# Kernel optimization log

Measured on AMD Instinct MI355X. Metric: run time of the kernel, lower is better.

The kernel has to match this reference:

```python
import jax, jax.numpy as jnp
import numpy as np

TIMESTEPS = 1000
ZERO_W = 1.0
NONZERO_W = 1.0
VT_W = 1.0
VX_W = 1.0
VY_W = 1.0


def _holographic_transform(x, timesteps, transpose):
    """x: (B,1,H,W) -> (B,1,H,timesteps).
    For each nonzero pixel (h,w) with value v, write w (the column index) at
    time bin q = int(v*timesteps)-1 (negative q wraps, as torch's x[-1]=...).
    Torch iterates nonzeros in row-major order so on collisions the largest
    column index wins -> scatter-max reproduces that deterministically.
    """
    img = x[:, 0]
    if transpose:  # virtual_dim == 'x'
        img = jnp.swapaxes(img, 1, 2)
    B, H, W = img.shape
    q = (img * timesteps).astype(jnp.int32) - 1
    # zeros -> out-of-range index `timesteps`, dropped by mode='drop';
    # nonzeros: wrap -1 -> timesteps-1 like torch negative indexing
    q = jnp.where(img != 0, q % timesteps, timesteps)
    ycoord = jnp.broadcast_to(jnp.arange(W, dtype=x.dtype), (B, H, W))
    b_idx = jnp.arange(B)[:, None, None]
    h_idx = jnp.arange(H)[None, :, None]
    out = jnp.zeros((B, H, timesteps), x.dtype)
    out = out.at[b_idx, h_idx, q].max(ycoord, mode='drop')
    return out[:, None]


def _acb_mse(recon, target, zero_w, nonzero_w):
    zero_mask = target == 0
    d2 = (recon - target) ** 2
    c0 = zero_mask.sum()
    c1 = (~zero_mask).sum()
    # mean over each class; empty class (NaN in torch) -> 0
    l0 = jnp.where(c0 > 0, jnp.where(zero_mask, d2, 0.0).sum() / jnp.maximum(c0, 1), 0.0)
    l1 = jnp.where(c1 > 0, jnp.where(zero_mask, 0.0, d2).sum() / jnp.maximum(c1, 1), 0.0)
    return zero_w * l0 + nonzero_w * l1


def setup_inputs() -> dict:
    key = jax.random.key(0)
    k1, k2, k3, k4 = jax.random.split(key, 4)
    B, H, W = 32, 512, 512

    def sparse_img(kv, km):
        v = jax.random.uniform(kv, (B, 1, H, W), dtype=jnp.float32)
        keep = jax.random.uniform(km, (B, 1, H, W)) < 0.05
        return jnp.where(keep, v, 0.0)

    return {
        "reconstructed_image": sparse_img(k1, k2),
        "target_image": sparse_img(k3, k4),
    }


def reference(reconstructed_image, target_image):
    vt = _acb_mse(reconstructed_image, target_image, ZERO_W, NONZERO_W) * VT_W

    rx = _holographic_transform(reconstructed_image, TIMESTEPS, transpose=True)
    tx = _holographic_transform(target_image, TIMESTEPS, transpose=True)
    vx = _acb_mse(rx, tx, ZERO_W, NONZERO_W) * VX_W

    ry = _holographic_transform(reconstructed_image, TIMESTEPS, transpose=False)
    ty = _holographic_transform(target_image, TIMESTEPS, transpose=False)
    vy = _acb_mse(ry, ty, ZERO_W, NONZERO_W) * VY_W

    return vt + vx + vy
```

## Files before the change

### kernel.cpp

```cpp
#include <hip/hip_runtime.h>

#define TS 1000

__device__ __forceinline__ double wred(double v) {
#pragma unroll
    for (int o = 32; o > 0; o >>= 1) v += __shfl_down(v, o, 64);
    return v;
}

__device__ __forceinline__ void scat(unsigned* bins, float v, unsigned val) {
    if (v != 0.0f) {
        int q = (int)(v * 1000.0f) - 1;
        if (q < 0) q += TS;
        atomicMax(&bins[q], val);
    }
}

__global__ void kinit(double* acc, int n) {
    int i = blockIdx.x * blockDim.x + threadIdx.x;
    if (i < n) acc[i] = 0.0;
}

__global__ __launch_bounds__(256, 4) void kmain(const float* __restrict__ R,
                                                const float* __restrict__ T,
                                                double* __restrict__ acc,
                                                int ncopy_mask) {
    __shared__ unsigned bins[8000];
    const int tid = threadIdx.x;
    const uint4 z4 = make_uint4(0u, 0u, 0u, 0u);

    {
        uint4* p = (uint4*)bins;
        for (int i = tid; i < 2000; i += 256) p[i] = z4;
    }
    __syncthreads();

    const int lane = tid & 63, wv = tid >> 6;
    const int id = blockIdx.x;
    double* accrow = acc + (size_t)(id & ncopy_mask) * 16;

    double s0 = 0.0, ssum = 0.0;
    int c1 = 0;

    if ((id & 1) == 0) {
        const int kid = id >> 1;
        double t0 = 0.0, tsum = 0.0;
        int tc1 = 0;
        unsigned* bR = bins + wv * 2000;
        unsigned* bT = bR + 1000;
        uint4* r4 = (uint4*)bR;
        uint4* t4 = (uint4*)bT;
        for (int it = 0; it < 4; it++) {
            const size_t row = (size_t)kid * 16 + (size_t)(wv * 4 + it);
            const float4* R4 = (const float4*)(R + row * 512);
            const float4* T4 = (const float4*)(T + row * 512);
#pragma unroll
            for (int k = 0; k < 2; k++) {
                const int c = lane + k * 64;
                float4 rv = R4[c];
                float4 tv = T4[c];
                float rr[4] = {rv.x, rv.y, rv.z, rv.w};
                float tt[4] = {tv.x, tv.y, tv.z, tv.w};
#pragma unroll
                for (int j = 0; j < 4; j++) {
                    float a = rr[j], b = tt[j];
                    float d = a - b, d2 = d * d;
                    bool bz = (b == 0.0f);
                    tsum += (double)d2;
                    t0 += bz ? (double)d2 : 0.0;
                    tc1 += bz ? 0 : 1;
                    scat(bR, a, (unsigned)(c * 4 + j));
                    scat(bT, b, (unsigned)(c * 4 + j));
                }
            }
            __syncthreads();
            for (int g = lane; g < 250; g += 64) {
                uint4 rg = r4[g], tg = t4[g];
                r4[g] = z4;
                t4[g] = z4;
                if (rg.x | rg.y | rg.z | rg.w | tg.x | tg.y | tg.z | tg.w) {
                    unsigned ru[4] = {rg.x, rg.y, rg.z, rg.w};
                    unsigned tu[4] = {tg.x, tg.y, tg.z, tg.w};
#pragma unroll
                    for (int j = 0; j < 4; j++) {
                        float rb = (float)ru[j], tb = (float)tu[j];
                        float d = rb - tb, d2 = d * d;
                        bool tz = (tb == 0.0f);
                        ssum += (double)d2;
                        s0 += tz ? (double)d2 : 0.0;
                        c1 += tz ? 0 : 1;
                    }
                }
            }
            __syncthreads();
        }
        double v0 = wred(t0), v1 = wred(tsum), v2 = wred((double)tc1);
        double v3 = wred(s0), v4 = wred(ssum), v5 = wred((double)c1);
        if (lane == 0) {
            atomicAdd(&accrow[0], v0);
            atomicAdd(&accrow[1], v1);
            atomicAdd(&accrow[2], v2);
            atomicAdd(&accrow[3], v3);
            atomicAdd(&accrow[4], v4);
            atomicAdd(&accrow[5], v5);
        }
    } else {
        const int kid = id >> 1;
        const int b = kid >> 5;
        const int line = kid & 31;
        const float* Rb = R + (size_t)b * (512 * 512) + (size_t)line * 16;
        const float* Tb = T + (size_t)b * (512 * 512) + (size_t)line * 16;

        float4 ra[8], ta[8];
#pragma unroll
        for (int k = 0; k < 8; k++) {
            const int h = k * 64 + (tid >> 2);
            const int sub = (tid + k) & 3;
            const size_t off = (size_t)h * 512 + sub * 4;
            ra[k] = *(const float4*)(Rb + off);
            ta[k] = *(const float4*)(Tb + off);
        }

        uint4* r4 = (uint4*)bins;
        uint4* t4 = (uint4*)(bins + 4000);
#pragma unroll
        for (int p = 0; p < 4; p++) {
#pragma unroll
            for (int k = 0; k < 8; k++) {
                if (((tid + k) & 3) == p) {
                    const unsigned h = (unsigned)(k * 64 + (tid >> 2));
                    scat(bins + 0 * 1000, ra[k].x, h);
                    scat(bins + 1 * 1000, ra[k].y, h);
                    scat(bins + 2 * 1000, ra[k].z, h);
                    scat(bins + 3 * 1000, ra[k].w, h);
                    scat(bins + 4000 + 0 * 1000, ta[k].x, h);
                    scat(bins + 4000 + 1 * 1000, ta[k].y, h);
                    scat(bins + 4000 + 2 * 1000, ta[k].z, h);
                    scat(bins + 4000 + 3 * 1000, ta[k].w, h);
                }
            }
            __syncthreads();
            for (int g = tid; g < 1000; g += 256) {
                uint4 rg = r4[g], tg = t4[g];
                r4[g] = z4;
                t4[g] = z4;
                if (rg.x | rg.y | rg.z | rg.w | tg.x | tg.y | tg.z | tg.w) {
                    unsigned ru[4] = {rg.x, rg.y, rg.z, rg.w};
                    unsigned tu[4] = {tg.x, tg.y, tg.z, tg.w};
#pragma unroll
                    for (int j = 0; j < 4; j++) {
                        float rb = (float)ru[j], tb = (float)tu[j];
                        float d = rb - tb, d2 = d * d;
                        bool tz = (tb == 0.0f);
                        ssum += (double)d2;
                        s0 += tz ? (double)d2 : 0.0;
                        c1 += tz ? 0 : 1;
                    }
                }
            }
            __syncthreads();
        }
        double v3 = wred(s0), v4 = wred(ssum), v5 = wred((double)c1);
        if (lane == 0) {
            atomicAdd(&accrow[6], v3);
            atomicAdd(&accrow[7], v4);
            atomicAdd(&accrow[8], v5);
        }
    }
}

__global__ void kfin(const double* __restrict__ acc, float* __restrict__ out,
                     int ncopy) {
    const int lane = threadIdx.x;
    double v[9];
#pragma unroll
    for (int k = 0; k < 9; k++) v[k] = 0.0;
    if (lane < ncopy) {
#pragma unroll
        for (int k = 0; k < 9; k++) v[k] = acc[(size_t)lane * 16 + k];
    }
#pragma unroll
    for (int k = 0; k < 9; k++) {
#pragma unroll
        for (int o = 16; o > 0; o >>= 1) v[k] += __shfl_down(v[k], o, 64);
    }
    if (lane == 0) {
        const double NT = 8388608.0;
        const double NB = 16384000.0;
        double vt_c1 = v[2], vy_c1 = v[5], vx_c1 = v[8];
        double vt_c0 = NT - vt_c1, vy_c0 = NB - vy_c1, vx_c0 = NB - vx_c1;
        double vt_s1 = v[1] - v[0];
        double vy_s1 = v[4] - v[3];
        double vx_s1 = v[7] - v[6];
        double vt = (vt_c0 > 0.0 ? v[0] / vt_c0 : 0.0) +
                    (vt_c1 > 0.0 ? vt_s1 / vt_c1 : 0.0);
        double vy = (vy_c0 > 0.0 ? v[3] / vy_c0 : 0.0) +
                    (vy_c1 > 0.0 ? vy_s1 / vy_c1 : 0.0);
        double vx = (vx_c0 > 0.0 ? v[6] / vx_c0 : 0.0) +
                    (vx_c1 > 0.0 ? vx_s1 / vx_c1 : 0.0);
        out[0] = (float)(vt + vx + vy);
    }
}

extern "C" void kernel_launch(void* const* d_in, const int* in_sizes, int n_in,
                              void* d_out, int out_size, void* d_ws, size_t ws_size,
                              hipStream_t stream) {
    const float* R = (const float*)d_in[0];
    const float* T = (const float*)d_in[1];
    double* acc = (double*)d_ws;
    float* out = (float*)d_out;

    int ncopy = 16;
    while (ncopy > 1 && (size_t)ncopy * 16 * sizeof(double) > ws_size) ncopy >>= 1;

    hipLaunchKernelGGL(kinit, dim3(1), dim3(256), 0, stream, acc, ncopy * 16);
    hipLaunchKernelGGL(kmain, dim3(2048), dim3(256), 0, stream, R, T, acc, ncopy - 1);
    hipLaunchKernelGGL(kfin, dim3(1), dim3(64), 0, stream, acc, out, ncopy);
}
```

Before: 77.02 us.

## Drop block barriers in row path, prefetch rows, split double accumulators

Row-path blocks now let each wavefront zero and use its own private bin region. Block-wide barriers are replaced by per-wave lgkmcnt waits, and the next row's global loads are prefetched while the current row is scattered. Bins are cleared only when non-empty and not on the last pass, and the column path overlaps bin zeroing with its global loads. Double-precision accumulators are split into two chains to shorten dependency latency, and launch bounds are raised to allow more resident blocks. Relying on s_waitcnt for intra-wave LDS ordering is subtle and could be fragile on some compilers or hardware.

```diff
diff --git a/kernel.cpp b/kernel.cpp
--- a/kernel.cpp
+++ b/kernel.cpp
@@ -21,81 +21,93 @@
     if (i < n) acc[i] = 0.0;
 }
 
-__global__ __launch_bounds__(256, 4) void kmain(const float* __restrict__ R,
+__global__ __launch_bounds__(256, 5) void kmain(const float* __restrict__ R,
                                                 const float* __restrict__ T,
                                                 double* __restrict__ acc,
                                                 int ncopy_mask) {
     __shared__ unsigned bins[8000];
     const int tid = threadIdx.x;
-    const uint4 z4 = make_uint4(0u, 0u, 0u, 0u);
-
-    {
-        uint4* p = (uint4*)bins;
-        for (int i = tid; i < 2000; i += 256) p[i] = z4;
-    }
-    __syncthreads();
-
     const int lane = tid & 63, wv = tid >> 6;
     const int id = blockIdx.x;
+    const uint4 z4 = make_uint4(0u, 0u, 0u, 0u);
     double* accrow = acc + (size_t)(id & ncopy_mask) * 16;
 
-    double s0 = 0.0, ssum = 0.0;
+    double s0a = 0.0, s0b = 0.0, ssa = 0.0, ssb = 0.0;
     int c1 = 0;
 
     if ((id & 1) == 0) {
         const int kid = id >> 1;
-        double t0 = 0.0, tsum = 0.0;
-        int tc1 = 0;
         unsigned* bR = bins + wv * 2000;
         unsigned* bT = bR + 1000;
         uint4* r4 = (uint4*)bR;
         uint4* t4 = (uint4*)bT;
+        for (int g = lane; g < 500; g += 64) r4[g] = z4;
+
+        const float4* R4 = (const float4*)(R + (size_t)(kid * 16 + wv * 4) * 512);
+        const float4* T4 = (const float4*)(T + (size_t)(kid * 16 + wv * 4) * 512);
+        double t0a = 0.0, t0b = 0.0, tsa = 0.0, tsb = 0.0;
+        int tc1 = 0;
+
+        float4 rv0 = R4[lane], rv1 = R4[lane + 64];
+        float4 tv0 = T4[lane], tv1 = T4[lane + 64];
+#pragma unroll
         for (int it = 0; it < 4; it++) {
-            const size_t row = (size_t)kid * 16 + (size_t)(wv * 4 + it);
-            const float4* R4 = (const float4*)(R + row * 512);
-            const float4* T4 = (const float4*)(T + row * 512);
-#pragma unroll
-            for (int k = 0; k < 2; k++) {
-                const int c = lane + k * 64;
-                float4 rv = R4[c];
-                float4 tv = T4[c];
-                float rr[4] = {rv.x, rv.y, rv.z, rv.w};
-                float tt[4] = {tv.x, tv.y, tv.z, tv.w};
-#pragma unroll
-                for (int j = 0; j < 4; j++) {
-                    float a = rr[j], b = tt[j];
-                    float d = a - b, d2 = d * d;
-                    bool bz = (b == 0.0f);
-                    tsum += (double)d2;
-                    t0 += bz ? (double)d2 : 0.0;
-                    tc1 += bz ? 0 : 1;
-                    scat(bR, a, (unsigned)(c * 4 + j));
-                    scat(bT, b, (unsigned)(c * 4 + j));
-                }
-            }
-            __syncthreads();
+            float4 nrv0, nrv1, ntv0, ntv1;
+            if (it < 3) {
+                const int o = (it + 1) * 128;
+                nrv0 = R4[o + lane];
+                nrv1 = R4[o + lane + 64];
+                ntv0 = T4[o + lane];
+                ntv1 = T4[o + lane + 64];
+            }
+            asm volatile("s_waitcnt lgkmcnt(0)" ::: "memory");
+            float rr[8] = {rv0.x, rv0.y, rv0.z, rv0.w, rv1.x, rv1.y, rv1.z, rv1.w};
+            float tt[8] = {tv0.x, tv0.y, tv0.z, tv0.w, tv1.x, tv1.y, tv1.z, tv1.w};
+#pragma unroll
+            for (int j = 0; j < 8; j++) {
+                float a = rr[j], b = tt[j];
+                float d = a - b, d2 = d * d;
+                bool bz = (b == 0.0f);
+                if (j & 1) {
+                    tsb += (double)d2;
+                    t0b += bz ? (double)d2 : 0.0;
+                } else {
+                    tsa += (double)d2;
+                    t0a += bz ? (double)d2 : 0.0;
+                }
+                tc1 += bz ? 0 : 1;
+                const unsigned w = (unsigned)((j < 4 ? lane : lane + 64) * 4 + (j & 3));
+                scat(bR, a, w);
+                scat(bT, b, w);
+            }
+            asm volatile("s_waitcnt lgkmcnt(0)" ::: "memory");
             for (int g = lane; g < 250; g += 64) {
                 uint4 rg = r4[g], tg = t4[g];
-                r4[g] = z4;
-                t4[g] = z4;
-                if (rg.x | rg.y | rg.z | rg.w | tg.x | tg.y | tg.z | tg.w) {
+                unsigned any = rg.x | rg.y | rg.z | rg.w | tg.x | tg.y | tg.z | tg.w;
+                if (any) {
+                    if (it < 3) { r4[g] = z4; t4[g] = z4; }
                     unsigned ru[4] = {rg.x, rg.y, rg.z, rg.w};
                     unsigned tu[4] = {tg.x, tg.y, tg.z, tg.w};
 #pragma unroll
-                    for (int j = 0; j < 4; j++) {
-                        float rb = (float)ru[j], tb = (float)tu[j];
+                    for (int j2 = 0; j2 < 4; j2++) {
+                        float rb = (float)ru[j2], tb = (float)tu[j2];
                         float d = rb - tb, d2 = d * d;
                         bool tz = (tb == 0.0f);
-                        ssum += (double)d2;
-                        s0 += tz ? (double)d2 : 0.0;
+                        if (j2 & 1) {
+                            ssb += (double)d2;
+                            s0b += tz ? (double)d2 : 0.0;
+                        } else {
+                            ssa += (double)d2;
+                            s0a += tz ? (double)d2 : 0.0;
+                        }
                         c1 += tz ? 0 : 1;
                     }
                 }
             }
-            __syncthreads();
-        }
-        double v0 = wred(t0), v1 = wred(tsum), v2 = wred((double)tc1);
-        double v3 = wred(s0), v4 = wred(ssum), v5 = wred((double)c1);
+            if (it < 3) { rv0 = nrv0; rv1 = nrv1; tv0 = ntv0; tv1 = ntv1; }
+        }
+        double v0 = wred(t0a + t0b), v1 = wred(tsa + tsb), v2 = wred((double)tc1);
+        double v3 = wred(s0a + s0b), v4 = wred(ssa + ssb), v5 = wred((double)c1);
         if (lane == 0) {
             atomicAdd(&accrow[0], v0);
             atomicAdd(&accrow[1], v1);
@@ -111,6 +123,11 @@
         const float* Rb = R + (size_t)b * (512 * 512) + (size_t)line * 16;
         const float* Tb = T + (size_t)b * (512 * 512) + (size_t)line * 16;
 
+        {
+            uint4* p = (uint4*)bins;
+            for (int i = tid; i < 2000; i += 256) p[i] = z4;
+        }
+
         float4 ra[8], ta[8];
 #pragma unroll
         for (int k = 0; k < 8; k++) {
@@ -120,11 +137,13 @@
             ra[k] = *(const float4*)(Rb + off);
             ta[k] = *(const float4*)(Tb + off);
         }
+        __syncthreads();
 
         uint4* r4 = (uint4*)bins;
         uint4* t4 = (uint4*)(bins + 4000);
 #pragma unroll
         for (int p = 0; p < 4; p++) {
+            if (p > 0) __syncthreads();
 #pragma unroll
             for (int k = 0; k < 8; k++) {
                 if (((tid + k) & 3) == p) {
@@ -142,9 +161,9 @@
             __syncthreads();
             for (int g = tid; g < 1000; g += 256) {
                 uint4 rg = r4[g], tg = t4[g];
-                r4[g] = z4;
-                t4[g] = z4;
-                if (rg.x | rg.y | rg.z | rg.w | tg.x | tg.y | tg.z | tg.w) {
+                unsigned any = rg.x | rg.y | rg.z | rg.w | tg.x | tg.y | tg.z | tg.w;
+                if (any) {
+                    if (p < 3) { r4[g] = z4; t4[g] = z4; }
                     unsigned ru[4] = {rg.x, rg.y, rg.z, rg.w};
                     unsigned tu[4] = {tg.x, tg.y, tg.z, tg.w};
 #pragma unroll
@@ -152,15 +171,19 @@
                         float rb = (float)ru[j], tb = (float)tu[j];
                         float d = rb - tb, d2 = d * d;
                         bool tz = (tb == 0.0f);
-                        ssum += (double)d2;
-                        s0 += tz ? (double)d2 : 0.0;
+                        if (j & 1) {
+                            ssb += (double)d2;
+                            s0b += tz ? (double)d2 : 0.0;
+                        } else {
+                            ssa += (double)d2;
+                            s0a += tz ? (double)d2 : 0.0;
+                        }
                         c1 += tz ? 0 : 1;
                     }
                 }
             }
-            __syncthreads();
-        }
-        double v3 = wred(s0), v4 = wred(ssum), v5 = wred((double)c1);
+        }
+        double v3 = wred(s0a + s0b), v4 = wred(ssa + ssb), v5 = wred((double)c1);
         if (lane == 0) {
             atomicAdd(&accrow[6], v3);
             atomicAdd(&accrow[7], v4);
```

Result: slower. 91.90 us (+19.3%).
